# Kernel tuning notes

Measured on AMD Instinct MI355X. Metric: run time of the kernel, lower is better.

The kernel has to match this reference:

```python
import jax, jax.numpy as jnp
import numpy as np

B, C, H, W = 4, 256, 64, 64
HID = C // 2


def setup_inputs() -> dict:
    key = jax.random.key(0)
    kx, kp, kt, kg, km = jax.random.split(key, 5)
    return {
        "x": jax.random.normal(kx, (B, C, H, W), dtype=jnp.float32),
        "w_phi": jax.random.normal(kp, (HID, C), dtype=jnp.float32) * 0.02,
        "w_theta": jax.random.normal(kt, (HID, C), dtype=jnp.float32) * 0.02,
        "w_g": jax.random.normal(kg, (HID, C), dtype=jnp.float32) * 0.02,
        "w_mask": jax.random.normal(km, (C, HID), dtype=jnp.float32) * 0.02,
    }


def reference(x, w_phi, w_theta, w_g, w_mask):
    b, c, h, w = x.shape
    n = h * w
    xf = x.reshape(b, c, n)                     # [B,C,N]
    # 1x1 convs == channel GEMMs
    phi = jnp.einsum('oc,bcn->bon', w_phi, xf)      # [B,HID,N]
    theta = jnp.einsum('oc,bcn->bon', w_theta, xf)  # [B,HID,N]
    g = jnp.einsum('oc,bcn->bon', w_g, xf)          # [B,HID,N]
    # attn[b,n,m] = sum_c theta[b,c,n] * phi[b,c,m]   (theta^T @ phi)
    attn = jnp.einsum('bcn,bcm->bnm', theta, phi)   # [B,N,N]
    # Faithful to nn.Softmax(dim=1): normalize over axis 1 (theta index)
    attn = jax.nn.softmax(attn, axis=1)
    # attn_g[b,n,c] = sum_m attn[b,n,m] * g[b,c,m]   (attn @ g^T)
    attn_g = jnp.einsum('bnm,bcm->bcn', attn, g)    # [B,HID,N] (already transposed back)
    mask = jnp.einsum('oc,bcn->bon', w_mask, attn_g).reshape(b, c, h, w)
    return mask + x
```

## Files before the change

### kernel.cpp

```cpp
#include <hip/hip_runtime.h>


#define NB   4
#define CIN  256
#define HIDN 128
#define NPIX 4096

typedef __attribute__((ext_vector_type(8))) short short8;
typedef __attribute__((ext_vector_type(4))) float f32x4;
typedef __attribute__((ext_vector_type(16))) float f32x16;

__device__ __forceinline__ unsigned short f2bf(float f) {
    unsigned u = __builtin_bit_cast(unsigned, f);
    u += 0x7fffu + ((u >> 16) & 1u);
    return (unsigned short)(u >> 16);
}
__device__ __forceinline__ unsigned f2bf2(float lo, float hi) {
    return (unsigned)f2bf(lo) | ((unsigned)f2bf(hi) << 16);
}
__device__ __forceinline__ float bf2f(unsigned short s) {
    return __builtin_bit_cast(float, (unsigned)s << 16);
}
__device__ __forceinline__ void cp16(void* lds, const void* g) {
    __builtin_amdgcn_global_load_lds(
        (const __attribute__((address_space(1))) unsigned int*)g,
        (__attribute__((address_space(3))) unsigned int*)lds, 16, 0, 0);
}

__global__ __launch_bounds__(256) void k_prep_w(
    const float* __restrict__ wp, const float* __restrict__ wt,
    const float* __restrict__ wg, const float* __restrict__ wm,
    unsigned short* __restrict__ Wp, unsigned short* __restrict__ Wt,
    unsigned short* __restrict__ Wg, unsigned short* __restrict__ Wm)
{
    const int which = blockIdx.x >> 3;
    const float* src = (which == 0) ? wp : (which == 1) ? wt : (which == 2) ? wg : wm;
    unsigned short* dst = (which == 0) ? Wp : (which == 1) ? Wt : (which == 2) ? Wg : Wm;
#pragma unroll
    for (int t = 0; t < 2; ++t) {
        const int gidx = ((blockIdx.x & 7) * 256 + threadIdx.x) * 2 + t;
        int o, srcc, dstc;
        if (which < 3) {
            o = gidx >> 5;
            const int gc = gidx & 31;
            const int sg = (gc & ~15) | ((gc & 15) ^ (o & 15));
            srcc = o * 256 + gc * 8; dstc = o * 256 + sg * 8;
        } else {
            o = gidx >> 4;
            const int gc = gidx & 15;
            const int sg = gc ^ (o & 15);
            srcc = o * 128 + gc * 8; dstc = o * 128 + sg * 8;
        }
        float4 a = *(const float4*)&src[srcc];
        float4 b = *(const float4*)&src[srcc + 4];
        uint4 v;
        v.x = f2bf2(a.x, a.y); v.y = f2bf2(a.z, a.w);
        v.z = f2bf2(b.x, b.y); v.w = f2bf2(b.z, b.w);
        *(uint4*)&dst[dstc] = v;
    }
}

__global__ __launch_bounds__(256) void k_prep_x(
    const float* __restrict__ x,
    unsigned short* __restrict__ xT,
    float* __restrict__ colsum)
{
    const int nt = blockIdx.x, ct = blockIdx.y, b = blockIdx.z;
    const int tid = threadIdx.x;
    if (ct == 0 && tid < 64) colsum[(size_t)b * NPIX + nt * 64 + tid] = 0.f;

    __shared__ unsigned short Ls[64][66];
    {
        const int c_loc = tid >> 2, n_seg = (tid & 3) * 16;
        const float* src = x + ((size_t)(b * CIN + ct * 64 + c_loc)) * NPIX + nt * 64 + n_seg;
#pragma unroll
        for (int j = 0; j < 8; ++j)
            *(unsigned*)&Ls[c_loc][n_seg + 2 * j] = f2bf2(src[2 * j], src[2 * j + 1]);
    }
    __syncthreads();
    {
        const int n_loc = tid >> 2, c_seg = (tid & 3) * 16;
        const int n_glob = nt * 64 + n_loc;
        unsigned short tmp[16];
#pragma unroll
        for (int j = 0; j < 16; ++j) tmp[j] = Ls[c_seg + j][n_loc];
#pragma unroll
        for (int gr = 0; gr < 2; ++gr) {
            const int c_base = ct * 64 + c_seg + gr * 8;
            const int sec = c_base >> 7;
            const int sg = (((c_base >> 3) & 15) ^ (n_glob & 15));
            *(uint4*)&xT[((size_t)b * NPIX + n_glob) * CIN + sec * 128 + sg * 8] =
                *(uint4*)&tmp[gr * 8];
        }
    }
}

__global__ __launch_bounds__(256, 3) void k_proj(
    const unsigned short* __restrict__ Wp,
    const unsigned short* __restrict__ Wt,
    const unsigned short* __restrict__ Wg,
    const unsigned short* __restrict__ xT,
    unsigned short* __restrict__ phiT,
    unsigned short* __restrict__ thetaT,
    unsigned short* __restrict__ gbuf)
{
    const int nt = blockIdx.x, ot = blockIdx.y, b = blockIdx.z;
    const unsigned short* W = (ot == 0) ? Wp : (ot == 1) ? Wt : Wg;

    __shared__ alignas(16) unsigned short Aw[128][128];
    __shared__ alignas(16) unsigned short Bx[64][128];

    const int tid = threadIdx.x;
    const int wave = tid >> 6, lane = tid & 63;
    const int oh = wave >> 1, nh = wave & 1;
    const int l31 = lane & 31, lh = lane >> 5;
    const int key = l31 & 15;

    f32x16 acc[2];
#pragma unroll
    for (int r = 0; r < 16; ++r) { acc[0][r] = 0.f; acc[1][r] = 0.f; }

    for (int kh = 0; kh < 2; ++kh) {
        __syncthreads();
#pragma unroll
        for (int i = 0; i < 8; ++i) {
            const int u = i * 256 + tid;
            cp16(&Aw[0][0] + u * 8, W + (u >> 4) * 256 + kh * 128 + (u & 15) * 8);
        }
#pragma unroll
        for (int i = 0; i < 4; ++i) {
            const int u = i * 256 + tid;
            cp16(&Bx[0][0] + u * 8,
                 xT + ((size_t)b * NPIX + nt * 64 + (u >> 4)) * CIN + kh * 128 + (u & 15) * 8);
        }
        __syncthreads();
#pragma unroll
        for (int ks = 0; ks < 8; ++ks) {
            const int g = ((ks * 2 + lh) ^ key) << 3;
            short8 bb = *(const short8*)&Bx[nh * 32 + l31][g];
#pragma unroll
            for (int t = 0; t < 2; ++t) {
                short8 a = *(const short8*)&Aw[oh * 64 + t * 32 + l31][g];
                acc[t] = __builtin_amdgcn_mfma_f32_32x32x16_bf16(a, bb, acc[t], 0, 0, 0);
            }
        }
    }

    const int n_glob = nt * 64 + nh * 32 + l31;
    if (ot < 2) {
        unsigned short* T = (ot == 0) ? phiT : thetaT;
#pragma unroll
        for (int t = 0; t < 2; ++t)
#pragma unroll
            for (int rg = 0; rg < 4; ++rg) {
                const int ob = oh * 64 + t * 32 + 8 * rg + 4 * lh;
                const int sc = (((ob >> 3) ^ (n_glob & 15)) << 3) | (ob & 7);
                uint2 v;
                v.x = f2bf2(acc[t][rg * 4 + 0], acc[t][rg * 4 + 1]);
                v.y = f2bf2(acc[t][rg * 4 + 2], acc[t][rg * 4 + 3]);
                *(uint2*)&T[((size_t)b * NPIX + n_glob) * HIDN + sc] = v;
            }
    } else {
        const int sbase = n_glob & ~127;
        const int g16 = (n_glob >> 3) & 15, c7off = n_glob & 7;
#pragma unroll
        for (int t = 0; t < 2; ++t)
#pragma unroll
            for (int r = 0; r < 16; ++r) {
                const int c = oh * 64 + t * 32 + (r & 3) + 8 * (r >> 2) + 4 * lh;
                const int sc = sbase | ((g16 ^ (c & 15)) << 3) | c7off;
                gbuf[((size_t)b * HIDN + c) * NPIX + sc] = f2bf(acc[t][r]);
            }
    }
}

__global__ __launch_bounds__(256, 3) void k_colsum(
    const unsigned short* __restrict__ thetaT,
    const unsigned short* __restrict__ phiT,
    float* __restrict__ colsum,
    float* __restrict__ O32)
{
    const int mt = blockIdx.x, ng = blockIdx.y, b = blockIdx.z;
    const int tid = threadIdx.x;
    {
        const int blin = ((blockIdx.z * 8 + blockIdx.y) * 32 + blockIdx.x);
        float* p = O32 + (size_t)blin * 2048 + tid * 8;
        *(f32x4*)p = f32x4{0.f, 0.f, 0.f, 0.f};
        *(f32x4*)(p + 4) = f32x4{0.f, 0.f, 0.f, 0.f};
    }

    __shared__ alignas(16) unsigned short As[2][64][128];

    const int wave = tid >> 6, lane = tid & 63;
    const int wn = wave & 1, wh = wave >> 1;
    const int l31 = lane & 31, lh = lane >> 5;
    const int key = l31 & 15;

    short8 bfrag[2][8];
#pragma unroll
    for (int t = 0; t < 2; ++t) {
        const int m = mt * 128 + wn * 64 + t * 32 + l31;
        const unsigned short* src = phiT + ((size_t)b * NPIX + m) * HIDN;
#pragma unroll
        for (int ks = 0; ks < 8; ++ks)
            bfrag[t][ks] = *(const short8*)(src + (((ks * 2 + lh) ^ key) << 3));
    }

#pragma unroll
    for (int i = 0; i < 4; ++i) {
        const int u = i * 256 + tid;
        cp16(&As[0][0][0] + u * 8,
             thetaT + ((size_t)b * NPIX + ng * 512 + (u >> 4)) * HIDN + (u & 15) * 8);
    }

    float csum[2] = {0.f, 0.f};

    for (int nc = 0; nc < 8; ++nc) {
        const int cur = nc & 1;
        __syncthreads();
        if (nc < 7) {
            const int n1 = ng * 512 + (nc + 1) * 64;
#pragma unroll
            for (int i = 0; i < 4; ++i) {
                const int u = i * 256 + tid;
                cp16(&As[cur ^ 1][0][0] + u * 8,
                     thetaT + ((size_t)b * NPIX + n1 + (u >> 4)) * HIDN + (u & 15) * 8);
            }
        }

        f32x16 acc[2];
#pragma unroll
        for (int r = 0; r < 16; ++r) { acc[0][r] = 0.f; acc[1][r] = 0.f; }
#pragma unroll
        for (int ks = 0; ks < 8; ++ks) {
            short8 a = *(const short8*)&As[cur][wh * 32 + l31][(((ks * 2 + lh) ^ key) << 3)];
            acc[0] = __builtin_amdgcn_mfma_f32_32x32x16_bf16(a, bfrag[0][ks], acc[0], 0, 0, 0);
            acc[1] = __builtin_amdgcn_mfma_f32_32x32x16_bf16(a, bfrag[1][ks], acc[1], 0, 0, 0);
        }
#pragma unroll
        for (int t = 0; t < 2; ++t)
#pragma unroll
            for (int r = 0; r < 16; ++r) csum[t] += __expf(acc[t][r]);
    }

#pragma unroll
    for (int t = 0; t < 2; ++t) {
        float s = csum[t];
        s += __shfl_xor(s, 32);
        if (lh == 0)
            atomicAdd(&colsum[(size_t)b * NPIX + mt * 128 + wn * 64 + t * 32 + l31], s);
    }
}

__global__ __launch_bounds__(256) void k_scale_g(
    unsigned short* __restrict__ gbuf, const float* __restrict__ colsum)
{
    const int idx = blockIdx.x * 256 + threadIdx.x;
    const int row = idx >> 9;
    const int sc = (idx & 511) * 8;
    const int bb = row >> 7;
    const int mt = (sc & ~127) | ((((sc >> 3) & 15) ^ (row & 15)) << 3);
    uint4 v = *(uint4*)&gbuf[(size_t)row * NPIX + sc];
    float4 c0 = *(const float4*)&colsum[(size_t)bb * NPIX + mt];
    float4 c1 = *(const float4*)&colsum[(size_t)bb * NPIX + mt + 4];
    unsigned short* vs = (unsigned short*)&v;
    const float cs[8] = {c0.x, c0.y, c0.z, c0.w, c1.x, c1.y, c1.z, c1.w};
#pragma unroll
    for (int j = 0; j < 8; ++j) vs[j] = f2bf(bf2f(vs[j]) / cs[j]);
    *(uint4*)&gbuf[(size_t)row * NPIX + sc] = v;
}

__global__ __launch_bounds__(256, 2) void k_attn(
    const unsigned short* __restrict__ thetaT,
    const unsigned short* __restrict__ phiT,
    const unsigned short* __restrict__ gbuf,
    float* __restrict__ O32)
{
    const int nt = blockIdx.x, ms = blockIdx.y, b = blockIdx.z;
    const int n0 = nt * 64;

    __shared__ alignas(16) unsigned short Gs[2][128][128];
    __shared__ alignas(16) unsigned short Ps[64][128];

    const int tid = threadIdx.x;
    const int wave = tid >> 6, lane = tid & 63;
    const int q = wave;
    const int nh = wave >> 1, ch = wave & 1;
    const int l31 = lane & 31, lh = lane >> 5;
    const int key = l31 & 15;

    short8 tfrag[2][8];
#pragma unroll
    for (int t = 0; t < 2; ++t) {
        const unsigned short* src =
            thetaT + ((size_t)b * NPIX + n0 + t * 32 + l31) * HIDN;
#pragma unroll
        for (int ks = 0; ks < 8; ++ks)
            tfrag[t][ks] = *(const short8*)(src + (((ks * 2 + lh) ^ key) << 3));
    }
    short8 pcur[8], pnxt[8];
    {
        const unsigned short* src =
            phiT + ((size_t)b * NPIX + ms * 2048 + q * 32 + l31) * HIDN;
#pragma unroll
        for (int ks = 0; ks < 8; ++ks)
            pcur[ks] = *(const short8*)(src + (((ks * 2 + lh) ^ key) << 3));
    }
#pragma unroll
    for (int i = 0; i < 8; ++i) {
        const int u = i * 256 + tid;
        cp16(&Gs[0][0][0] + u * 8,
             gbuf + ((size_t)b * HIDN + (u >> 4)) * NPIX + ms * 2048 + (u & 15) * 8);
    }

    f32x16 accO[2];
#pragma unroll
    for (int r = 0; r < 16; ++r) { accO[0][r] = 0.f; accO[1][r] = 0.f; }

    for (int mc = 0; mc < 16; ++mc) {
        const int cur = mc & 1;
        const int m0 = ms * 2048 + mc * 128;

        f32x16 accS[2];
#pragma unroll
        for (int r = 0; r < 16; ++r) { accS[0][r] = 0.f; accS[1][r] = 0.f; }
#pragma unroll
        for (int ks = 0; ks < 8; ++ks) {
            accS[0] = __builtin_amdgcn_mfma_f32_32x32x16_bf16(pcur[ks], tfrag[0][ks], accS[0], 0, 0, 0);
            accS[1] = __builtin_amdgcn_mfma_f32_32x32x16_bf16(pcur[ks], tfrag[1][ks], accS[1], 0, 0, 0);
        }
        if (mc < 15) {
            const unsigned short* src =
                phiT + ((size_t)b * NPIX + m0 + 128 + q * 32 + l31) * HIDN;
#pragma unroll
            for (int ks = 0; ks < 8; ++ks)
                pnxt[ks] = *(const short8*)(src + (((ks * 2 + lh) ^ key) << 3));
        }
#pragma unroll
        for (int t = 0; t < 2; ++t) {
            const int n = t * 32 + l31;
#pragma unroll
            for (int rg = 0; rg < 4; ++rg) {
                uint2 v;
                v.x = f2bf2(__expf(accS[t][rg * 4 + 0]), __expf(accS[t][rg * 4 + 1]));
                v.y = f2bf2(__expf(accS[t][rg * 4 + 2]), __expf(accS[t][rg * 4 + 3]));
                const int gm = q * 4 + rg;
                const int col = ((gm ^ (n & 15)) << 3) | (4 * lh);
                *(uint2*)&Ps[n][col] = v;
            }
        }
        __syncthreads();
        if (mc < 15) {
#pragma unroll
            for (int i = 0; i < 8; ++i) {
                const int u = i * 256 + tid;
                cp16(&Gs[cur ^ 1][0][0] + u * 8,
                     gbuf + ((size_t)b * HIDN + (u >> 4)) * NPIX + m0 + 128 + (u & 15) * 8);
            }
        }
#pragma unroll
        for (int ks = 0; ks < 8; ++ks) {
            const int g = ((ks * 2 + lh) ^ key) << 3;
            short8 pa = *(const short8*)&Ps[nh * 32 + l31][g];
            short8 g0 = *(const short8*)&Gs[cur][ch * 64 + l31][g];
            short8 g1 = *(const short8*)&Gs[cur][ch * 64 + 32 + l31][g];
            accO[0] = __builtin_amdgcn_mfma_f32_32x32x16_bf16(pa, g0, accO[0], 0, 0, 0);
            accO[1] = __builtin_amdgcn_mfma_f32_32x32x16_bf16(pa, g1, accO[1], 0, 0, 0);
        }
        __syncthreads();

#pragma unroll
        for (int ks = 0; ks < 8; ++ks) pcur[ks] = pnxt[ks];
    }

#pragma unroll
    for (int t = 0; t < 2; ++t)
#pragma unroll
        for (int r = 0; r < 16; ++r) {
            const int n = n0 + nh * 32 + (r & 3) + 8 * (r >> 2) + 4 * lh;
            const int c = ch * 64 + t * 32 + l31;
            atomicAdd(&O32[((size_t)b * NPIX + n) * HIDN + c], accO[t][r]);
        }
}

__global__ __launch_bounds__(256, 3) void k_mask(
    const unsigned short* __restrict__ Wm,
    const float* __restrict__ O32,
    const float* __restrict__ x,
    float* __restrict__ out)
{
    const int nt = blockIdx.x, ct = blockIdx.y, b = blockIdx.z;
    __shared__ alignas(16) unsigned short As[128][128];
    __shared__ alignas(16) unsigned short Bs[64][128];

    const int tid = threadIdx.x;
    const int wave = tid >> 6, lane = tid & 63;
    const int oh = wave >> 1, nh = wave & 1;
    const int l31 = lane & 31, lh = lane >> 5;
    const int key = l31 & 15;

#pragma unroll
    for (int i = 0; i < 8; ++i) {
        const int u = i * 256 + tid;
        cp16(&As[0][0] + u * 8, Wm + (ct * 128 + (u >> 4)) * HIDN + (u & 15) * 8);
    }
    {
        const int n_loc = tid >> 2, seg = (tid & 3) * 32;
        const float* src = O32 + ((size_t)b * NPIX + nt * 64 + n_loc) * HIDN + seg;
        const int k7 = n_loc & 7;
#pragma unroll
        for (int j = 0; j < 4; ++j) {
            const int gr = (seg >> 3) + j;
            const int sg = (gr & ~7) | ((gr & 7) ^ k7);
            const float* s8 = src + j * 8;
            unsigned* d = (unsigned*)&Bs[n_loc][sg * 8];
#pragma unroll
            for (int k = 0; k < 4; ++k) d[k] = f2bf2(s8[2 * k], s8[2 * k + 1]);
        }
    }
    __syncthreads();

    f32x16 acc[2];
#pragma unroll
    for (int r = 0; r < 16; ++r) { acc[0][r] = 0.f; acc[1][r] = 0.f; }
#pragma unroll
    for (int ks = 0; ks < 8; ++ks) {
        const int gr = ks * 2 + lh;
        const int sgb = ((gr & ~7) | ((gr & 7) ^ (l31 & 7))) << 3;
        short8 bb = *(const short8*)&Bs[nh * 32 + l31][sgb];
#pragma unroll
        for (int t = 0; t < 2; ++t) {
            short8 a = *(const short8*)&As[oh * 64 + t * 32 + l31][((gr ^ key) << 3)];
            acc[t] = __builtin_amdgcn_mfma_f32_32x32x16_bf16(a, bb, acc[t], 0, 0, 0);
        }
    }

    const int n = nt * 64 + nh * 32 + l31;
#pragma unroll
    for (int t = 0; t < 2; ++t)
#pragma unroll
        for (int r = 0; r < 16; ++r) {
            const int co = ct * 128 + oh * 64 + t * 32 + (r & 3) + 8 * (r >> 2) + 4 * lh;
            const size_t idx = ((size_t)b * CIN + co) * NPIX + n;
            out[idx] = acc[t][r] + x[idx];
        }
}

extern "C" void kernel_launch(void* const* d_in, const int* in_sizes, int n_in,
                              void* d_out, int out_size, void* d_ws, size_t ws_size,
                              hipStream_t stream)
{
    (void)in_sizes; (void)n_in; (void)out_size; (void)ws_size;
    const float* x       = (const float*)d_in[0];
    const float* w_phi   = (const float*)d_in[1];
    const float* w_theta = (const float*)d_in[2];
    const float* w_g     = (const float*)d_in[3];
    const float* w_mask  = (const float*)d_in[4];
    float* out = (float*)d_out;

    char* ws = (char*)d_ws;
    unsigned short* phiT   = (unsigned short*)(ws);
    unsigned short* thetaT = (unsigned short*)(ws + 4194304);
    unsigned short* gbuf   = (unsigned short*)(ws + 8388608);
    float*          colsum = (float*)(ws + 12582912);
    unsigned short* xT     = (unsigned short*)(ws + 12648448);
    float*          O32    = (float*)(ws + 12648448);
    unsigned short* Wp     = (unsigned short*)(ws + 21037056);
    unsigned short* Wt     = (unsigned short*)(ws + 21102592);
    unsigned short* Wg     = (unsigned short*)(ws + 21168128);
    unsigned short* Wm     = (unsigned short*)(ws + 21233664);

    k_prep_w <<<dim3(32),        256, 0, stream>>>(w_phi, w_theta, w_g, w_mask, Wp, Wt, Wg, Wm);
    k_prep_x <<<dim3(64, 4, 4),  256, 0, stream>>>(x, xT, colsum);
    k_proj   <<<dim3(64, 3, 4),  256, 0, stream>>>(Wp, Wt, Wg, xT, phiT, thetaT, gbuf);
    k_colsum <<<dim3(32, 8, 4),  256, 0, stream>>>(thetaT, phiT, colsum, O32);
    k_scale_g<<<dim3(1024),      256, 0, stream>>>(gbuf, colsum);
    k_attn   <<<dim3(64, 2, 4),  256, 0, stream>>>(thetaT, phiT, gbuf, O32);
    k_mask   <<<dim3(64, 2, 4),  256, 0, stream>>>(Wm, O32, x, out);
}
```

Baseline: 169.5 us.

## Load G fragments directly to registers, double-buffer P, use exp2 and packed bf16 converts

The attention kernel stops staging g in shared memory through async global-to-LDS copies. Each wave now loads its phi and g MFMA fragments straight from global memory into registers on every chunk. The P tile is double-buffered in LDS, which removes the second barrier per iteration. Theta is pre-scaled by log2(e) so the softmax exponentials can use the hardware exp2, and bf16 rounding goes through the packed convert builtin when it is available. The trade-off is more redundant global and L2 traffic, higher register pressure, and no prefetch overlap of the loads with the MFMAs.

Result: slower. 187.1 us (+10.4%).

```diff
diff --git a/kernel.cpp b/kernel.cpp
--- a/kernel.cpp
+++ b/kernel.cpp
@@ -17,6 +17,22 @@
 }
 __device__ __forceinline__ unsigned f2bf2(float lo, float hi) {
     return (unsigned)f2bf(lo) | ((unsigned)f2bf(hi) << 16);
+}
+__device__ __forceinline__ unsigned pk2bf(float lo, float hi) {
+#if __has_builtin(__builtin_amdgcn_cvt_pk_bf16_f32)
+    typedef __attribute__((ext_vector_type(2))) __bf16 bf16x2;
+    bf16x2 v = __builtin_amdgcn_cvt_pk_bf16_f32(lo, hi);
+    return __builtin_bit_cast(unsigned, v);
+#else
+    return f2bf2(lo, hi);
+#endif
+}
+__device__ __forceinline__ float fexp2(float x) {
+#if __has_builtin(__builtin_amdgcn_exp2f)
+    return __builtin_amdgcn_exp2f(x);
+#else
+    return exp2f(x);
+#endif
 }
 __device__ __forceinline__ float bf2f(unsigned short s) {
     return __builtin_bit_cast(float, (unsigned)s << 16);
@@ -54,8 +70,8 @@
         float4 a = *(const float4*)&src[srcc];
         float4 b = *(const float4*)&src[srcc + 4];
         uint4 v;
-        v.x = f2bf2(a.x, a.y); v.y = f2bf2(a.z, a.w);
-        v.z = f2bf2(b.x, b.y); v.w = f2bf2(b.z, b.w);
+        v.x = pk2bf(a.x, a.y); v.y = pk2bf(a.z, a.w);
+        v.z = pk2bf(b.x, b.y); v.w = pk2bf(b.z, b.w);
         *(uint4*)&dst[dstc] = v;
     }
 }
@@ -75,7 +91,7 @@
         const float* src = x + ((size_t)(b * CIN + ct * 64 + c_loc)) * NPIX + nt * 64 + n_seg;
 #pragma unroll
         for (int j = 0; j < 8; ++j)
-            *(unsigned*)&Ls[c_loc][n_seg + 2 * j] = f2bf2(src[2 * j], src[2 * j + 1]);
+            *(unsigned*)&Ls[c_loc][n_seg + 2 * j] = pk2bf(src[2 * j], src[2 * j + 1]);
     }
     __syncthreads();
     {
@@ -149,6 +165,7 @@
     const int n_glob = nt * 64 + nh * 32 + l31;
     if (ot < 2) {
         unsigned short* T = (ot == 0) ? phiT : thetaT;
+        const float osc = (ot == 1) ? 1.4426950408889634f : 1.0f;
 #pragma unroll
         for (int t = 0; t < 2; ++t)
 #pragma unroll
@@ -156,8 +173,8 @@
                 const int ob = oh * 64 + t * 32 + 8 * rg + 4 * lh;
                 const int sc = (((ob >> 3) ^ (n_glob & 15)) << 3) | (ob & 7);
                 uint2 v;
-                v.x = f2bf2(acc[t][rg * 4 + 0], acc[t][rg * 4 + 1]);
-                v.y = f2bf2(acc[t][rg * 4 + 2], acc[t][rg * 4 + 3]);
+                v.x = pk2bf(acc[t][rg * 4 + 0] * osc, acc[t][rg * 4 + 1] * osc);
+                v.y = pk2bf(acc[t][rg * 4 + 2] * osc, acc[t][rg * 4 + 3] * osc);
                 *(uint2*)&T[((size_t)b * NPIX + n_glob) * HIDN + sc] = v;
             }
     } else {
@@ -240,7 +257,7 @@
 #pragma unroll
         for (int t = 0; t < 2; ++t)
 #pragma unroll
-            for (int r = 0; r < 16; ++r) csum[t] += __expf(acc[t][r]);
+            for (int r = 0; r < 16; ++r) csum[t] += fexp2(acc[t][r]);
     }
 
 #pragma unroll
@@ -279,8 +296,7 @@
     const int nt = blockIdx.x, ms = blockIdx.y, b = blockIdx.z;
     const int n0 = nt * 64;
 
-    __shared__ alignas(16) unsigned short Gs[2][128][128];
-    __shared__ alignas(16) unsigned short Ps[64][128];
+    __shared__ alignas(16) unsigned short Ps[2][64][128];
 
     const int tid = threadIdx.x;
     const int wave = tid >> 6, lane = tid & 63;
@@ -298,20 +314,12 @@
         for (int ks = 0; ks < 8; ++ks)
             tfrag[t][ks] = *(const short8*)(src + (((ks * 2 + lh) ^ key) << 3));
     }
-    short8 pcur[8], pnxt[8];
-    {
-        const unsigned short* src =
-            phiT + ((size_t)b * NPIX + ms * 2048 + q * 32 + l31) * HIDN;
-#pragma unroll
-        for (int ks = 0; ks < 8; ++ks)
-            pcur[ks] = *(const short8*)(src + (((ks * 2 + lh) ^ key) << 3));
-    }
-#pragma unroll
-    for (int i = 0; i < 8; ++i) {
-        const int u = i * 256 + tid;
-        cp16(&Gs[0][0][0] + u * 8,
-             gbuf + ((size_t)b * HIDN + (u >> 4)) * NPIX + ms * 2048 + (u & 15) * 8);
-    }
+
+    const unsigned short* pphi =
+        phiT + ((size_t)b * NPIX + ms * 2048 + q * 32 + l31) * HIDN;
+    const unsigned short* pg0 =
+        gbuf + ((size_t)b * HIDN + ch * 64 + l31) * NPIX + ms * 2048;
+    const unsigned short* pg1 = pg0 + 32 * NPIX;
 
     f32x16 accO[2];
 #pragma unroll
@@ -319,22 +327,24 @@
 
     for (int mc = 0; mc < 16; ++mc) {
         const int cur = mc & 1;
-        const int m0 = ms * 2048 + mc * 128;
+
+        short8 pf[8], gf[2][8];
+#pragma unroll
+        for (int ks = 0; ks < 8; ++ks) {
+            const int go = ((ks * 2 + lh) ^ key) << 3;
+            pf[ks]    = *(const short8*)(pphi + go);
+            gf[0][ks] = *(const short8*)(pg0 + go);
+            gf[1][ks] = *(const short8*)(pg1 + go);
+        }
+        pphi += 128 * HIDN; pg0 += 128; pg1 += 128;
 
         f32x16 accS[2];
 #pragma unroll
         for (int r = 0; r < 16; ++r) { accS[0][r] = 0.f; accS[1][r] = 0.f; }
 #pragma unroll
         for (int ks = 0; ks < 8; ++ks) {
-            accS[0] = __builtin_amdgcn_mfma_f32_32x32x16_bf16(pcur[ks], tfrag[0][ks], accS[0], 0, 0, 0);
-            accS[1] = __builtin_amdgcn_mfma_f32_32x32x16_bf16(pcur[ks], tfrag[1][ks], accS[1], 0, 0, 0);
-        }
-        if (mc < 15) {
-            const unsigned short* src =
-                phiT + ((size_t)b * NPIX + m0 + 128 + q * 32 + l31) * HIDN;
-#pragma unroll
-            for (int ks = 0; ks < 8; ++ks)
-                pnxt[ks] = *(const short8*)(src + (((ks * 2 + lh) ^ key) << 3));
+            accS[0] = __builtin_amdgcn_mfma_f32_32x32x16_bf16(pf[ks], tfrag[0][ks], accS[0], 0, 0, 0);
+            accS[1] = __builtin_amdgcn_mfma_f32_32x32x16_bf16(pf[ks], tfrag[1][ks], accS[1], 0, 0, 0);
         }
 #pragma unroll
         for (int t = 0; t < 2; ++t) {
@@ -342,35 +352,22 @@
 #pragma unroll
             for (int rg = 0; rg < 4; ++rg) {
                 uint2 v;
-                v.x = f2bf2(__expf(accS[t][rg * 4 + 0]), __expf(accS[t][rg * 4 + 1]));
-                v.y = f2bf2(__expf(accS[t][rg * 4 + 2]), __expf(accS[t][rg * 4 + 3]));
+                v.x = pk2bf(fexp2(accS[t][rg * 4 + 0]), fexp2(accS[t][rg * 4 + 1]));
+                v.y = pk2bf(fexp2(accS[t][rg * 4 + 2]), fexp2(accS[t][rg * 4 + 3]));
                 const int gm = q * 4 + rg;
                 const int col = ((gm ^ (n & 15)) << 3) | (4 * lh);
-                *(uint2*)&Ps[n][col] = v;
+                *(uint2*)&Ps[cur][n][col] = v;
             }
         }
         __syncthreads();
-        if (mc < 15) {
-#pragma unroll
-            for (int i = 0; i < 8; ++i) {
-                const int u = i * 256 + tid;
-                cp16(&Gs[cur ^ 1][0][0] + u * 8,
-                     gbuf + ((size_t)b * HIDN + (u >> 4)) * NPIX + m0 + 128 + (u & 15) * 8);
-            }
-        }
+
 #pragma unroll
         for (int ks = 0; ks < 8; ++ks) {
             const int g = ((ks * 2 + lh) ^ key) << 3;
-            short8 pa = *(const short8*)&Ps[nh * 32 + l31][g];
-            short8 g0 = *(const short8*)&Gs[cur][ch * 64 + l31][g];
-            short8 g1 = *(const short8*)&Gs[cur][ch * 64 + 32 + l31][g];
-            accO[0] = __builtin_amdgcn_mfma_f32_32x32x16_bf16(pa, g0, accO[0], 0, 0, 0);
-            accO[1] = __builtin_amdgcn_mfma_f32_32x32x16_bf16(pa, g1, accO[1], 0, 0, 0);
-        }
-        __syncthreads();
-
-#pragma unroll
-        for (int ks = 0; ks < 8; ++ks) pcur[ks] = pnxt[ks];
+            short8 pa = *(const short8*)&Ps[cur][nh * 32 + l31][g];
+            accO[0] = __builtin_amdgcn_mfma_f32_32x32x16_bf16(pa, gf[0][ks], accO[0], 0, 0, 0);
+            accO[1] = __builtin_amdgcn_mfma_f32_32x32x16_bf16(pa, gf[1][ks], accO[1], 0, 0, 0);
+        }
     }
 
 #pragma unroll
@@ -415,7 +412,7 @@
             const float* s8 = src + j * 8;
             unsigned* d = (unsigned*)&Bs[n_loc][sg * 8];
 #pragma unroll
-            for (int k = 0; k < 4; ++k) d[k] = f2bf2(s8[2 * k], s8[2 * k + 1]);
+            for (int k = 0; k < 4; ++k) d[k] = pk2bf(s8[2 * k], s8[2 * k + 1]);
         }
     }
     __syncthreads();
```
